# Performance work log

Hardware: AMD Instinct MI355X
Metric: run time of the kernel (lower is better)

## Reference

```python
import jax, jax.numpy as jnp
import numpy as np

DATASET_SIZE = 202599  # CelebA
BETA = 6.0
LOG2PI = float(np.log(2.0 * np.pi))


def gaussian_log_likelihood(x, mean, log_var):
    # elementwise Gaussian log density
    return -0.5 * (LOG2PI + log_var + jnp.square(x - mean) * jnp.exp(-log_var))


def setup_inputs() -> dict:
    key = jax.random.key(0)
    ks = jax.random.split(key, 6)
    B, D, L = 256, 12288, 32
    return {
        "target": jax.random.uniform(ks[0], (B, D), dtype=jnp.float32),
        "x_mean": jax.random.normal(ks[1], (B, D), dtype=jnp.float32),
        "x_log_var": jax.random.normal(ks[2], (B, D), dtype=jnp.float32),
        "z": jax.random.normal(ks[3], (B, L), dtype=jnp.float32),
        "z_mean": jax.random.normal(ks[4], (B, L), dtype=jnp.float32),
        "z_log_var": jax.random.normal(ks[5], (B, L), dtype=jnp.float32),
    }


def reference(target, x_mean, x_log_var, z, z_mean, z_log_var):
    B = target.shape[0]
    log_nm = jnp.log(jnp.float32(B * DATASET_SIZE))

    # reconstruction log-likelihood, [B]
    log_px = jnp.sum(gaussian_log_likelihood(target, x_mean, x_log_var), axis=1)
    # prior N(0, I), [B]
    log_pz = jnp.sum(gaussian_log_likelihood(z, 0.0, 0.0), axis=1)
    # posterior q(z|x), [B]
    log_qzx = jnp.sum(gaussian_log_likelihood(z, z_mean, z_log_var), axis=1)

    # pairwise log q(z_i | x_j): [B, B, L]
    # NOTE: faithful to original: mean expanded on axis=1, log_var on axis=0.
    log_qz_matrix = gaussian_log_likelihood(
        z[:, None, :], z_mean[:, None, :][None].squeeze(0) if False else jnp.expand_dims(z_mean, 1),
        jnp.expand_dims(z_log_var, 0))

    # product of marginals term, [B]
    log_qz_prod = jnp.sum(jax.nn.logsumexp(log_qz_matrix, axis=1) - log_nm, axis=1)
    # aggregate posterior, [B]
    log_qz = jax.nn.logsumexp(jnp.sum(log_qz_matrix, axis=2), axis=1) - log_nm

    mutual_information = log_qzx - log_qz
    total_correlation = log_qz - log_qz_prod
    kld = log_qz_prod - log_pz

    loss = -jnp.mean(log_px - mutual_information - BETA * total_correlation - kld, axis=0)
    return loss
```

## Files before the change

kernel.cpp:

```cpp
#include <hip/hip_runtime.h>
#include <math.h>

#define BB 256
#define DD 12288
#define LL 32
#define NPXB 1536
#define LOG2PI_F 1.8378770664093453f
#define BETA_F 6.0f


__global__ __launch_bounds__(256) void tcvae_main(
    const float* __restrict__ target,
    const float* __restrict__ x_mean,
    const float* __restrict__ x_log_var,
    const float* __restrict__ z,
    const float* __restrict__ z_mean,
    const float* __restrict__ z_log_var,
    float* __restrict__ ws, float log_nm)
{
    const int tid = threadIdx.x;
    const int bid = blockIdx.x;

    __shared__ float ch[8][257];
    __shared__ float red[8];
    __shared__ float lse_l[LL];
    __shared__ float sd2[LL];
    __shared__ float misc[2];

    const int wid = tid >> 6, lane = tid & 63;

    if (bid >= BB) {
        const size_t base = (size_t)(bid - BB) * 512;
        const float4* t4 = (const float4*)target    + base;
        const float4* m4 = (const float4*)x_mean    + base;
        const float4* v4 = (const float4*)x_log_var + base;
        float4 x0 = t4[tid], x1 = t4[tid + 256];
        float4 m0 = m4[tid], m1 = m4[tid + 256];
        float4 l0 = v4[tid], l1 = v4[tid + 256];
        float dx, acc = 0.f;
        dx = x0.x - m0.x; acc += l0.x + dx * dx * __expf(-l0.x);
        dx = x0.y - m0.y; acc += l0.y + dx * dx * __expf(-l0.y);
        dx = x0.z - m0.z; acc += l0.z + dx * dx * __expf(-l0.z);
        dx = x0.w - m0.w; acc += l0.w + dx * dx * __expf(-l0.w);
        dx = x1.x - m1.x; acc += l1.x + dx * dx * __expf(-l1.x);
        dx = x1.y - m1.y; acc += l1.y + dx * dx * __expf(-l1.y);
        dx = x1.z - m1.z; acc += l1.z + dx * dx * __expf(-l1.z);
        dx = x1.w - m1.w; acc += l1.w + dx * dx * __expf(-l1.w);
        #pragma unroll
        for (int o = 32; o; o >>= 1) acc += __shfl_xor(acc, o, 64);
        if (lane == 0) red[wid] = acc;
        __syncthreads();
        if (tid == 0) ws[bid - BB] = red[0] + red[1] + red[2] + red[3];
        return;
    }

    const int i = bid;

    if (tid < 64) {
        float pz = 0.f, qzx = 0.f;
        if (tid < LL) {
            float zl  = z[i * LL + tid];
            float zm  = z_mean[i * LL + tid];
            float lvi = z_log_var[i * LL + tid];
            float d   = zl - zm;
            float d2  = d * d;
            sd2[tid]  = d2;
            pz  = -0.5f * (LOG2PI_F + zl * zl);
            qzx = -0.5f * (LOG2PI_F + lvi + d2 * __expf(-lvi));
        }
        #pragma unroll
        for (int o = 32; o; o >>= 1) {
            pz  += __shfl_xor(pz,  o, 64);
            qzx += __shfl_xor(qzx, o, 64);
        }
        if (tid == 0) { misc[0] = pz; misc[1] = qzx; }
    }
    __syncthreads();

    const int j = tid;
    const float4* lv4 = (const float4*)(z_log_var + j * LL);
    float mv[32];
    float s_j = 0.f;
    #pragma unroll
    for (int qq = 0; qq < 8; ++qq) {
        float4 lv = lv4[qq];
        const int l0i = qq * 4;
        float A, e, v;
        A = -0.5f * (LOG2PI_F + lv.x); e = __expf(-lv.x);
        v = A - 0.5f * sd2[l0i + 0] * e; mv[l0i + 0] = v; s_j += v;
        A = -0.5f * (LOG2PI_F + lv.y); e = __expf(-lv.y);
        v = A - 0.5f * sd2[l0i + 1] * e; mv[l0i + 1] = v; s_j += v;
        A = -0.5f * (LOG2PI_F + lv.z); e = __expf(-lv.z);
        v = A - 0.5f * sd2[l0i + 2] * e; mv[l0i + 2] = v; s_j += v;
        A = -0.5f * (LOG2PI_F + lv.w); e = __expf(-lv.w);
        v = A - 0.5f * sd2[l0i + 3] * e; mv[l0i + 3] = v; s_j += v;
    }

    float mx = s_j;
    #pragma unroll
    for (int o = 32; o; o >>= 1) mx = fmaxf(mx, __shfl_xor(mx, o, 64));
    if (lane == 0) red[wid] = mx;
    __syncthreads();
    mx = fmaxf(fmaxf(red[0], red[1]), fmaxf(red[2], red[3]));
    float es = __expf(s_j - mx);
    #pragma unroll
    for (int o = 32; o; o >>= 1) es += __shfl_xor(es, o, 64);
    if (lane == 0) red[4 + wid] = es;
    __syncthreads();
    const float log_qz = mx + __logf(red[4] + red[5] + red[6] + red[7]) - log_nm;

    const int lrow = tid >> 5;
    const int k    = tid & 31;
    #pragma unroll
    for (int c = 0; c < 4; ++c) {
        __syncthreads();
        #pragma unroll
        for (int r = 0; r < 8; ++r) ch[r][j] = mv[c * 8 + r];
        __syncthreads();
        float vv[8];
        float m2 = -INFINITY;
        #pragma unroll
        for (int mm = 0; mm < 8; ++mm) {
            vv[mm] = ch[lrow][k + 32 * mm];
            m2 = fmaxf(m2, vv[mm]);
        }
        #pragma unroll
        for (int o = 16; o; o >>= 1) m2 = fmaxf(m2, __shfl_xor(m2, o, 64));
        float se = 0.f;
        #pragma unroll
        for (int mm = 0; mm < 8; ++mm) se += __expf(vv[mm] - m2);
        #pragma unroll
        for (int o = 16; o; o >>= 1) se += __shfl_xor(se, o, 64);
        if (k == 0) lse_l[c * 8 + lrow] = m2 + __logf(se);
    }
    __syncthreads();

    if (tid < 64) {
        float v = (tid < LL) ? lse_l[tid] : 0.f;
        #pragma unroll
        for (int o = 32; o; o >>= 1) v += __shfl_xor(v, o, 64);
        if (tid == 0) {
            const float log_qz_prod = v - (float)LL * log_nm;
            const float t = misc[0] - misc[1]
                          + (1.f - BETA_F) * log_qz
                          + (BETA_F - 1.f) * log_qz_prod;
            ws[2048 + i] = t;
        }
    }
}

__global__ __launch_bounds__(64) void tcvae_final(
    const float* __restrict__ ws, float* __restrict__ out)
{
    const int lane = threadIdx.x;
    const float4* w4 = (const float4*)ws;
    const float4* t4 = (const float4*)(ws + 2048);
    float s = 0.f;
    #pragma unroll
    for (int q = 0; q < 6; ++q) {
        float4 w = w4[lane + 64 * q];
        s += w.x + w.y + w.z + w.w;
    }
    float4 tt = t4[lane];
    float t = tt.x + tt.y + tt.z + tt.w;
    #pragma unroll
    for (int o = 32; o; o >>= 1) {
        s += __shfl_xor(s, o, 64);
        t += __shfl_xor(t, o, 64);
    }
    if (lane == 0) {
        const float log_px_sum = -0.5f * ((float)BB * (float)DD * LOG2PI_F + s);
        out[0] = -(log_px_sum + t) * (1.0f / (float)BB);
    }
}

extern "C" void kernel_launch(void* const* d_in, const int* in_sizes, int n_in,
                              void* d_out, int out_size, void* d_ws, size_t ws_size,
                              hipStream_t stream) {
    const float* target    = (const float*)d_in[0];
    const float* x_mean    = (const float*)d_in[1];
    const float* x_log_var = (const float*)d_in[2];
    const float* z         = (const float*)d_in[3];
    const float* z_mean    = (const float*)d_in[4];
    const float* z_log_var = (const float*)d_in[5];
    float* ws  = (float*)d_ws;
    float* out = (float*)d_out;

    const float log_nm = logf((float)BB * 202599.0f);

    tcvae_main<<<BB + NPXB, 256, 0, stream>>>(target, x_mean, x_log_var,
                                              z, z_mean, z_log_var, ws, log_nm);
    tcvae_final<<<1, 64, 0, stream>>>(ws, out);
}
```

Before: 15.21 us.

## Fuse final reduction into main kernel via atomics and use nontemporal loads

Removes the second finalize kernel by having each block atomically add its scaled partial contribution straight into the output, which is zeroed with a memset beforehand. The constant log(2π) term is folded in by block 0. Streaming loads of the large reconstruction tensors are switched to nontemporal loads. This saves a kernel launch and the workspace round-trip, but adds a memset call, 1792 float atomics to a single address, and a summation order that is no longer deterministic.

```diff
diff --git a/kernel.cpp b/kernel.cpp
--- a/kernel.cpp
+++ b/kernel.cpp
@@ -5,21 +5,25 @@
 #define DD 12288
 #define LL 32
 #define NPXB 1536
+#define GRID (NPXB + BB)
 #define LOG2PI_F 1.8378770664093453f
 #define BETA_F 6.0f
 
+typedef float f4 __attribute__((ext_vector_type(4)));
 
-__global__ __launch_bounds__(256) void tcvae_main(
+
+__global__ __launch_bounds__(256) void tcvae_one(
     const float* __restrict__ target,
     const float* __restrict__ x_mean,
     const float* __restrict__ x_log_var,
     const float* __restrict__ z,
     const float* __restrict__ z_mean,
     const float* __restrict__ z_log_var,
-    float* __restrict__ ws, float log_nm)
+    float* __restrict__ out, float log_nm)
 {
     const int tid = threadIdx.x;
     const int bid = blockIdx.x;
+    const int wid = tid >> 6, lane = tid & 63;
 
     __shared__ float ch[8][257];
     __shared__ float red[8];
@@ -27,16 +31,17 @@
     __shared__ float sd2[LL];
     __shared__ float misc[2];
 
-    const int wid = tid >> 6, lane = tid & 63;
-
     if (bid >= BB) {
         const size_t base = (size_t)(bid - BB) * 512;
-        const float4* t4 = (const float4*)target    + base;
-        const float4* m4 = (const float4*)x_mean    + base;
-        const float4* v4 = (const float4*)x_log_var + base;
-        float4 x0 = t4[tid], x1 = t4[tid + 256];
-        float4 m0 = m4[tid], m1 = m4[tid + 256];
-        float4 l0 = v4[tid], l1 = v4[tid + 256];
+        const f4* t4 = (const f4*)target    + base;
+        const f4* m4 = (const f4*)x_mean    + base;
+        const f4* v4 = (const f4*)x_log_var + base;
+        f4 x0 = __builtin_nontemporal_load(t4 + tid);
+        f4 x1 = __builtin_nontemporal_load(t4 + tid + 256);
+        f4 m0 = __builtin_nontemporal_load(m4 + tid);
+        f4 m1 = __builtin_nontemporal_load(m4 + tid + 256);
+        f4 l0 = __builtin_nontemporal_load(v4 + tid);
+        f4 l1 = __builtin_nontemporal_load(v4 + tid + 256);
         float dx, acc = 0.f;
         dx = x0.x - m0.x; acc += l0.x + dx * dx * __expf(-l0.x);
         dx = x0.y - m0.y; acc += l0.y + dx * dx * __expf(-l0.y);
@@ -50,7 +55,10 @@
         for (int o = 32; o; o >>= 1) acc += __shfl_xor(acc, o, 64);
         if (lane == 0) red[wid] = acc;
         __syncthreads();
-        if (tid == 0) ws[bid - BB] = red[0] + red[1] + red[2] + red[3];
+        if (tid == 0) {
+            const float s = red[0] + red[1] + red[2] + red[3];
+            atomicAdd(out, 0.5f * s * (1.0f / (float)BB));
+        }
         return;
     }
 
@@ -144,33 +152,10 @@
             const float t = misc[0] - misc[1]
                           + (1.f - BETA_F) * log_qz
                           + (BETA_F - 1.f) * log_qz_prod;
-            ws[2048 + i] = t;
+            float contrib = -t * (1.0f / (float)BB);
+            if (i == 0) contrib += 0.5f * (float)DD * LOG2PI_F;
+            atomicAdd(out, contrib);
         }
-    }
-}
-
-__global__ __launch_bounds__(64) void tcvae_final(
-    const float* __restrict__ ws, float* __restrict__ out)
-{
-    const int lane = threadIdx.x;
-    const float4* w4 = (const float4*)ws;
-    const float4* t4 = (const float4*)(ws + 2048);
-    float s = 0.f;
-    #pragma unroll
-    for (int q = 0; q < 6; ++q) {
-        float4 w = w4[lane + 64 * q];
-        s += w.x + w.y + w.z + w.w;
-    }
-    float4 tt = t4[lane];
-    float t = tt.x + tt.y + tt.z + tt.w;
-    #pragma unroll
-    for (int o = 32; o; o >>= 1) {
-        s += __shfl_xor(s, o, 64);
-        t += __shfl_xor(t, o, 64);
-    }
-    if (lane == 0) {
-        const float log_px_sum = -0.5f * ((float)BB * (float)DD * LOG2PI_F + s);
-        out[0] = -(log_px_sum + t) * (1.0f / (float)BB);
     }
 }
 
@@ -183,12 +168,12 @@
     const float* z         = (const float*)d_in[3];
     const float* z_mean    = (const float*)d_in[4];
     const float* z_log_var = (const float*)d_in[5];
-    float* ws  = (float*)d_ws;
     float* out = (float*)d_out;
 
     const float log_nm = logf((float)BB * 202599.0f);
 
-    tcvae_main<<<BB + NPXB, 256, 0, stream>>>(target, x_mean, x_log_var,
-                                              z, z_mean, z_log_var, ws, log_nm);
-    tcvae_final<<<1, 64, 0, stream>>>(ws, out);
+    (void)hipMemsetAsync(d_out, 0, sizeof(float), stream);
+
+    tcvae_one<<<GRID, 256, 0, stream>>>(target, x_mean, x_log_var,
+                                        z, z_mean, z_log_var, out, log_nm);
 }
```

Result: slower. 35.38 us (+132.6%).
